# Performance work log

Measured on AMD Instinct MI355X. Metric: run time of the kernel, lower is better.

## Reference

```python
import jax, jax.numpy as jnp
import numpy as np
import math

PERIODS = [4, 2, 1]          # period_num[-3:] sorted desc
SEQ, PRED, CH = 192, 96, 8
TOPM, DM = 20, 512
N_TRAIN, BSZ = 10000, 32


def decompose_mg(data):
    # data: [N, L, C] -> mg: [P, N, L, C], offset-removed (last step per period)
    N, L, C = data.shape
    mgs = []
    for g in PERIODS:
        cur = data.reshape(N, L // g, g, C).mean(axis=2)   # pooled
        cur = jnp.repeat(cur, g, axis=1)                   # repeat_interleave
        mgs.append(cur)
    mg = jnp.stack(mgs, axis=0)                            # [P, N, L, C]
    offset = mg[:, :, -1:, :]
    return mg - offset


def l2norm(x, eps=1e-12):
    n = jnp.sqrt(jnp.sum(x * x, axis=-1, keepdims=True))
    return x / jnp.maximum(n, eps)


def setup_inputs() -> dict:
    key = jax.random.key(0)
    ks = jax.random.split(key, 10)
    F = SEQ * CH
    return {
        "x": jax.random.normal(ks[0], (BSZ, SEQ, CH), dtype=jnp.float32),
        "index": jax.random.randint(ks[1], (BSZ,), 0, N_TRAIN),
        "train_data_all": jax.random.normal(ks[2], (N_TRAIN, SEQ, CH), dtype=jnp.float32),
        "y_data_all": jax.random.normal(ks[3], (N_TRAIN, PRED, CH), dtype=jnp.float32),
        "W_sim": jax.random.normal(ks[4], (F, F), dtype=jnp.float32) / math.sqrt(F),
        "b_sim": jax.random.normal(ks[5], (F,), dtype=jnp.float32) * 0.01,
        "Wq": jax.random.normal(ks[6], (CH, DM), dtype=jnp.float32) / math.sqrt(CH),
        "bq": jax.random.normal(ks[7], (DM,), dtype=jnp.float32) * 0.01,
        "Wk": jax.random.normal(ks[8], (CH, DM), dtype=jnp.float32) / math.sqrt(CH),
        "bk": jax.random.normal(ks[9], (DM,), dtype=jnp.float32) * 0.01,
    }


def reference(x, index, train_data_all, y_data_all, W_sim, b_sim, Wq, bq, Wk, bk):
    P = len(PERIODS)
    bsz = x.shape[0]
    n_train = train_data_all.shape[0]

    # multi-period decomposition (prepare_dataset + retrieve)
    train_mg = decompose_mg(train_data_all)   # [P, N, SEQ, CH]
    y_mg = decompose_mg(y_data_all)           # [P, N, PRED, CH]
    x_mg = decompose_mg(x)                    # [P, B, SEQ, CH]

    # periodic_batch_corr: shared linear then cosine similarity
    bx = x_mg.reshape(P, bsz, -1) @ W_sim + b_sim           # [P, B, F]
    ax = train_mg.reshape(P, n_train, -1) @ W_sim + b_sim   # [P, N, F]
    sim = jnp.einsum('pbf,pnf->pbn', l2norm(bx), l2norm(ax))

    # self-exclusion sliding mask (train=True)
    win = 2 * (SEQ + PRED) - 1
    slid = jnp.arange(win)[None, :] + (index - SEQ - PRED + 1)[:, None]
    slid = jnp.clip(slid, 0, n_train - 1)
    mask = jnp.zeros((bsz, n_train), dtype=bool).at[
        jnp.arange(bsz)[:, None], slid].set(True)
    sim = jnp.where(mask[None], -jnp.inf, sim)

    # top-m retrieval
    _, topm_idx = jax.lax.top_k(sim, TOPM)                  # [P, B, TOPM]

    # gather neighbors per period
    gather = jax.vmap(lambda src, i: src[i])                # over period axis
    k = gather(train_mg, topm_idx)                          # [P, B, M, SEQ, CH]
    v = gather(y_mg, topm_idx)                              # [P, B, M, PRED, CH]

    # cross attention (shared projections across periods)
    q_emb = x_mg @ Wq + bq                                  # [P, B, S, D]
    k_emb = k @ Wk + bk                                     # [P, B, M, T, D]
    scores = jnp.einsum('pbsd,pbmtd->pbsmt', q_emb, k_emb) / math.sqrt(DM)
    S = scores.shape[2]
    w = jax.nn.softmax(scores.reshape(P, bsz, S, TOPM * S), axis=-1)
    w = w.reshape(P, bsz, S, TOPM, S)
    nw = w.sum(axis=-1).sum(axis=2)                         # [P, B, M]
    nw = jax.nn.softmax(nw, axis=-1)
    out = jnp.einsum('pbm,pbmlc->pblc', nw, v)              # [P, B, PRED, CH]
    return out
```

## Files before the change

### kernel.cpp

```cpp
#include <hip/hip_runtime.h>
#include <hip/hip_bf16.h>
#include <math.h>

#define NPER 3
#define SEQL 192
#define PREDL 96
#define CH 8
#define FD 1536
#define NT 10000
#define BS 32
#define PB 96
#define TOPM 20
#define DM 512
#define HALFW 287
#define NROWS 30000
#define NRP2 10112
#define NRB2 79
#define NCB 12
#define PCOLS 24
#define NWG2 (NRB2*NCB)
#define NJ 3840
#define K0R 384
#define K1R 768
#define K2R 1536
#define KS 16
#define NCH 4
#define CHSZ (NT/NCH)
#define NWTG 4080
#define NB_DOT (3*NRB2)
#define BUFSZ (2*128*32)
#define RSQRT_DM 0.04419417382415922f

typedef __attribute__((ext_vector_type(8))) short bf16x8;
typedef __attribute__((ext_vector_type(4))) float f32x4;
typedef __attribute__((address_space(3))) short lds_short_t;
typedef __attribute__((address_space(1))) const short glb_short_t;

__device__ inline float bflo(unsigned u){ return __uint_as_float(u << 16); }
__device__ inline float bfhi(unsigned u){ return __uint_as_float(u & 0xFFFF0000u); }
__device__ inline float bf2f(unsigned short u){ return __uint_as_float((unsigned)u << 16); }
__device__ inline unsigned short f2bf(float v){
  __hip_bfloat16 h = __float2bfloat16(v);
  return *reinterpret_cast<unsigned short*>(&h);
}

template<int L>
__device__ __forceinline__ void dec_body(const float* __restrict__ data,
                                         float* __restrict__ mg,
                                         __hip_bfloat16* __restrict__ m0,
                                         __hip_bfloat16* __restrict__ m1,
                                         __hip_bfloat16* __restrict__ m2,
                                         __hip_bfloat16* __restrict__ trH,
                                         __hip_bfloat16* __restrict__ trL,
                                         int N, int n, float* fpool) {
  float* row = fpool;
  float* m4  = fpool + L*CH;
  float* m2s = fpool + L*CH + (L/4)*CH;
  const float* src = data + (size_t)n*L*CH;
  for (int e = threadIdx.x; e < L*CH/4; e += 256)
    *reinterpret_cast<float4*>(&row[e*4]) = *reinterpret_cast<const float4*>(&src[e*4]);
  __syncthreads();
  for (int i = threadIdx.x; i < (L/4)*CH; i += 256) {
    int j = i >> 3, c = i & 7;
    m4[i] = (row[(4*j)*CH+c] + row[(4*j+1)*CH+c] + row[(4*j+2)*CH+c] + row[(4*j+3)*CH+c]) * 0.25f;
  }
  for (int i = threadIdx.x; i < (L/2)*CH; i += 256) {
    int j = i >> 3, c = i & 7;
    m2s[i] = (row[(2*j)*CH+c] + row[(2*j+1)*CH+c]) * 0.5f;
  }
  __syncthreads();
  if (mg) {
    size_t plane = (size_t)N*L*CH;
    size_t base  = (size_t)n*L*CH;
    for (int e = threadIdx.x; e < L*CH/4; e += 256) {
      int i = e*4;
      int l = i >> 3, c0 = i & 7;
      float v0[4], v1[4], v2[4];
      #pragma unroll
      for (int j=0;j<4;j++) {
        int c = c0 + j;
        v0[j] = m4[(l>>2)*CH+c] - m4[(L/4-1)*CH+c];
        v1[j] = m2s[(l>>1)*CH+c] - m2s[(L/2-1)*CH+c];
        v2[j] = row[i+j] - row[(L-1)*CH+c];
      }
      *reinterpret_cast<float4*>(&mg[base+i])           = make_float4(v0[0],v0[1],v0[2],v0[3]);
      *reinterpret_cast<float4*>(&mg[plane+base+i])     = make_float4(v1[0],v1[1],v1[2],v1[3]);
      *reinterpret_cast<float4*>(&mg[2*plane+base+i])   = make_float4(v2[0],v2[1],v2[2],v2[3]);
    }
  }
  if (m0) {
    unsigned short* p0 = (unsigned short*)m0 + (size_t)n*K0R;
    unsigned short* p1 = (unsigned short*)m1 + (size_t)n*K1R;
    unsigned short* p2 = (unsigned short*)m2 + (size_t)n*K2R;
    for (int e = threadIdx.x; e < K0R/4; e += 256) {
      int i = e*4, c0 = i & 7;
      ushort4 u;
      u.x = f2bf(m4[i]   - m4[(L/4-1)*CH + c0]);
      u.y = f2bf(m4[i+1] - m4[(L/4-1)*CH + c0+1]);
      u.z = f2bf(m4[i+2] - m4[(L/4-1)*CH + c0+2]);
      u.w = f2bf(m4[i+3] - m4[(L/4-1)*CH + c0+3]);
      *reinterpret_cast<ushort4*>(&p0[i]) = u;
    }
    for (int e = threadIdx.x; e < K1R/4; e += 256) {
      int i = e*4, c0 = i & 7;
      ushort4 u;
      u.x = f2bf(m2s[i]   - m2s[(L/2-1)*CH + c0]);
      u.y = f2bf(m2s[i+1] - m2s[(L/2-1)*CH + c0+1]);
      u.z = f2bf(m2s[i+2] - m2s[(L/2-1)*CH + c0+2]);
      u.w = f2bf(m2s[i+3] - m2s[(L/2-1)*CH + c0+3]);
      *reinterpret_cast<ushort4*>(&p1[i]) = u;
    }
    for (int e = threadIdx.x; e < K2R/4; e += 256) {
      int i = e*4, c0 = i & 7;
      ushort4 u;
      u.x = f2bf(row[i]   - row[(L-1)*CH + c0]);
      u.y = f2bf(row[i+1] - row[(L-1)*CH + c0+1]);
      u.z = f2bf(row[i+2] - row[(L-1)*CH + c0+2]);
      u.w = f2bf(row[i+3] - row[(L-1)*CH + c0+3]);
      *reinterpret_cast<ushort4*>(&p2[i]) = u;
    }
  }
  if (trH) {
    unsigned short* h = (unsigned short*)trH + (size_t)n*L*CH;
    unsigned short* l = (unsigned short*)trL + (size_t)n*L*CH;
    for (int e = threadIdx.x; e < L*CH/4; e += 256) {
      int i = e*4;
      ushort4 uh, ul;
      uh.x = f2bf(row[i]);   ul.x = f2bf(row[i]   - bf2f(uh.x));
      uh.y = f2bf(row[i+1]); ul.y = f2bf(row[i+1] - bf2f(uh.y));
      uh.z = f2bf(row[i+2]); ul.z = f2bf(row[i+2] - bf2f(uh.z));
      uh.w = f2bf(row[i+3]); ul.w = f2bf(row[i+3] - bf2f(uh.w));
      *reinterpret_cast<ushort4*>(&h[i]) = uh;
      *reinterpret_cast<ushort4*>(&l[i]) = ul;
    }
  }
}

__device__ __forceinline__ void wtg_body(const float* __restrict__ W,
                                         __hip_bfloat16* __restrict__ wt0,
                                         __hip_bfloat16* __restrict__ wt1,
                                         __hip_bfloat16* __restrict__ wt2,
                                         const float* __restrict__ Wq,
                                         const float* __restrict__ bq,
                                         const float* __restrict__ Wk,
                                         const float* __restrict__ bk,
                                         float* __restrict__ cst,
                                         int wb, float* fpool) {
  int bxx = wb / 48, byy = wb % 48;
  if (bxx == 84) {
    if (byy != 0) return;
    int tt = threadIdx.x;
    if (tt < 64) {
      int c = tt >> 3, e = tt & 7;
      float s = 0.f;
      for (int d=0; d<DM; d++) s += Wq[c*DM+d] * Wk[e*DM+d];
      cst[tt] = s;
    } else if (tt < 72) {
      int c = tt - 64; float s=0.f;
      for (int d=0;d<DM;d++) s += Wq[c*DM+d]*bk[d];
      cst[tt] = s;
    } else if (tt < 80) {
      int e = tt - 72; float s=0.f;
      for (int d=0;d<DM;d++) s += Wk[e*DM+d]*bq[d];
      cst[tt] = s;
    } else if (tt == 80) {
      float s=0.f;
      for (int d=0;d<DM;d++) s += bq[d]*bk[d];
      cst[80] = s;
    }
    return;
  }
  int G, kr0, Kred;
  __hip_bfloat16* Wt;
  if (bxx < 12)      { G = 4; kr0 = bxx*32;      Kred = K0R; Wt = wt0; }
  else if (bxx < 36) { G = 2; kr0 = (bxx-12)*32; Kred = K1R; Wt = wt1; }
  else               { G = 1; kr0 = (bxx-36)*32; Kred = K2R; Wt = wt2; }
  int f0 = byy*32;
  int k0 = kr0*G;
  int tid = threadIdx.x, tx = tid & 31, ty = tid >> 5;
  for (int i = ty; i < 32*G; i += 8)
    fpool[i*33 + tx] = W[(size_t)(k0+i)*FD + f0 + tx];
  __syncthreads();
  for (int fl = ty; fl < 32; fl += 8) {
    float s = 0.f;
    for (int i=0;i<G;i++) s += fpool[(((tx>>3)*G+i)*8 + (tx&7))*33 + fl];
    Wt[(size_t)(f0+fl)*Kred + kr0 + tx] = __float2bfloat16(s);
  }
}

__global__ __launch_bounds__(256) void k_front(const float* __restrict__ x,
                                               const float* __restrict__ train,
                                               float* __restrict__ x_mg,
                                               __hip_bfloat16* __restrict__ m0,
                                               __hip_bfloat16* __restrict__ m1,
                                               __hip_bfloat16* __restrict__ m2,
                                               __hip_bfloat16* __restrict__ trH,
                                               __hip_bfloat16* __restrict__ trL,
                                               const float* __restrict__ W,
                                               __hip_bfloat16* __restrict__ wt0,
                                               __hip_bfloat16* __restrict__ wt1,
                                               __hip_bfloat16* __restrict__ wt2,
                                               const float* __restrict__ Wq,
                                               const float* __restrict__ bq,
                                               const float* __restrict__ Wk,
                                               const float* __restrict__ bk,
                                               float* __restrict__ cst) {
  __shared__ float fpool[128*33];
  int bid = blockIdx.x;
  if (bid < NT) {
    dec_body<SEQL>(train, nullptr, m0, m1, m2, trH, trL, NT, bid, fpool);
  } else if (bid < NT + NWTG) {
    wtg_body(W, wt0, wt1, wt2, Wq, bq, Wk, bk, cst, bid - NT, fpool);
  } else {
    dec_body<SEQL>(x, x_mg, nullptr, nullptr, nullptr, nullptr, nullptr,
                   BS, bid - NT - NWTG, fpool);
  }
}

__global__ __launch_bounds__(256) void k_bx_part(const float* __restrict__ xmg,
                                                 const float* __restrict__ W,
                                                 float* __restrict__ bxp) {
  __shared__ float xs[PB][17];
  __shared__ float Ws[16][65];
  int f0 = blockIdx.x * 64;
  int ks = blockIdx.y;
  int kbase = ks * (FD/KS);
  int tid = threadIdx.x;
  int fl = tid & 63, gp = tid >> 6;
  float acc[24];
  #pragma unroll
  for (int j=0;j<24;j++) acc[j]=0.f;
  for (int k0 = kbase; k0 < kbase + FD/KS; k0 += 16) {
    for (int e = tid; e < PB*16; e += 256) {
      int r = e >> 4, k = e & 15;
      xs[r][k] = xmg[(size_t)r*FD + k0 + k];
    }
    for (int e = tid; e < 16*64; e += 256) {
      int k = e >> 6, f = e & 63;
      Ws[k][f] = W[(size_t)(k0+k)*FD + f0 + f];
    }
    __syncthreads();
    #pragma unroll
    for (int kk = 0; kk < 16; kk++) {
      float w = Ws[kk][fl];
      #pragma unroll
      for (int j=0;j<24;j++) acc[j] += w * xs[gp + 4*j][kk];
    }
    __syncthreads();
  }
  #pragma unroll
  for (int j=0;j<24;j++) {
    int pb = gp + 4*j;
    bxp[((size_t)ks*PB + pb)*FD + f0 + fl] = acc[j];
  }
}

__global__ __launch_bounds__(256) void k_bxnorm(const float* __restrict__ bxp,
                                                const float* __restrict__ bsim,
                                                float* __restrict__ u_out,
                                                float* __restrict__ cpb) {
  __shared__ float rowv[FD];
  __shared__ float r1[256], r2[256];
  __shared__ float invs;
  int pb = blockIdx.x, tid = threadIdx.x;
  float s2 = 0.f, sb = 0.f;
  for (int f = tid; f < FD; f += 256) {
    float s = 0.f;
    #pragma unroll
    for (int ks=0; ks<KS; ks++) s += bxp[((size_t)ks*PB + pb)*FD + f];
    s += bsim[f];
    rowv[f] = s;
    s2 += s*s; sb += s*bsim[f];
  }
  r1[tid]=s2; r2[tid]=sb; __syncthreads();
  for (int off=128; off>0; off>>=1) {
    if (tid<off) { r1[tid]+=r1[tid+off]; r2[tid]+=r2[tid+off]; }
    __syncthreads();
  }
  if (tid==0) {
    float iv = 1.f / fmaxf(sqrtf(r1[0]), 1e-12f);
    invs = iv;
    cpb[pb] = r2[0] * iv;
  }
  __syncthreads();
  float iv = invs;
  for (int f = tid; f < FD; f += 256) u_out[(size_t)pb*FD + f] = rowv[f]*iv;
}

__global__ __launch_bounds__(256) void k_t_part(const float* __restrict__ u,
                                                const float* __restrict__ W,
                                                float* __restrict__ tp) {
  __shared__ float us[PB][17];
  __shared__ float Wt[64][17];
  int k0 = blockIdx.x * 64;
  int ks = blockIdx.y;
  int fbase = ks * (FD/KS);
  int tid = threadIdx.x;
  int kl = tid & 63, gp = tid >> 6;
  float acc[24];
  #pragma unroll
  for (int j=0;j<24;j++) acc[j]=0.f;
  for (int fc = fbase; fc < fbase + FD/KS; fc += 16) {
    for (int e = tid; e < PB*16; e += 256) {
      int r = e >> 4, f = e & 15;
      us[r][f] = u[(size_t)r*FD + fc + f];
    }
    for (int e = tid; e < 64*16; e += 256) {
      int k = e >> 4, f = e & 15;
      Wt[k][f] = W[(size_t)(k0+k)*FD + fc + f];
    }
    __syncthreads();
    #pragma unroll
    for (int ff = 0; ff < 16; ff++) {
      float w = Wt[kl][ff];
      #pragma unroll
      for (int j=0;j<24;j++) acc[j] += w * us[gp + 4*j][ff];
    }
    __syncthreads();
  }
  #pragma unroll
  for (int j=0;j<24;j++) {
    int pb = gp + 4*j;
    tp[((size_t)ks*PB + pb)*FD + k0 + kl] = acc[j];
  }
}

__global__ __launch_bounds__(192) void k_tred_adj(const float* __restrict__ tp,
                                                  __hip_bfloat16* __restrict__ tadjH,
                                                  __hip_bfloat16* __restrict__ tadjL) {
  __shared__ float ts[SEQL*CH];
  __shared__ float Tc[CH];
  int pb = blockIdx.x;
  int p = pb / BS;
  int g = (p==0) ? 4 : (p==1) ? 2 : 1;
  int l = threadIdx.x;
  #pragma unroll
  for (int c=0;c<CH;c++) {
    float s = 0.f;
    #pragma unroll
    for (int ks=0; ks<KS; ks++) s += tp[((size_t)ks*PB + pb)*FD + l*CH + c];
    ts[l*CH+c] = s;
  }
  __syncthreads();
  if (l < CH) {
    float s=0.f;
    for (int j=0;j<SEQL;j++) s += ts[j*CH+l];
    Tc[l] = s;
  }
  __syncthreads();
  int j0 = (l/g)*g;
  bool last = (j0 == SEQL-g);
  float ig = 1.f/(float)g;
  unsigned short* th = (unsigned short*)tadjH;
  unsigned short* tl = (unsigned short*)tadjL;
  #pragma unroll
  for (int c=0;c<CH;c++) {
    float s = 0.f;
    for (int jj=0;jj<g;jj++) s += ts[(j0+jj)*CH+c];
    float v = s*ig - (last ? Tc[c]*ig : 0.f);
    unsigned short hv = f2bf(v);
    th[(size_t)pb*FD + l*CH+c] = hv;
    tl[(size_t)pb*FD + l*CH+c] = f2bf(v - bf2f(hv));
  }
}

__device__ __forceinline__ void norm_body(const short* __restrict__ A,
                                          const short* __restrict__ B,
                                          int K, int p, int seg,
                                          const float* __restrict__ bsim,
                                          float* __restrict__ part,
                                          short* pool) {
  int q = NWG2 >> 3, r = NWG2 & 7;
  int xcd = seg & 7, pos = seg >> 3;
  int wgid = (xcd < r ? xcd*(q+1) : r*(q+1) + (xcd-r)*q) + pos;
  int rb = wgid / NCB, cb = wgid - rb*NCB;
  int row0 = rb*128, col0 = cb*128;
  int tid = threadIdx.x, lane = tid & 63, wid = tid >> 6;
  int wr = (wid>>1)*64, wc = (wid&1)*64;

  size_t aoff[2], boff[2];
  int ldsb[2];
  #pragma unroll
  for (int i=0;i<2;i++) {
    int lrow = (wid*2+i)*16 + (lane>>2);
    int sl = lane & 3;
    int ss = (sl - lrow - (lrow>>2)) & 3;
    aoff[i] = (size_t)(row0 + lrow)*K + 8*ss;
    boff[i] = (size_t)(col0 + lrow)*K + 8*ss;
    ldsb[i] = (wid*2+i)*16*32;
  }

  f32x4 acc[4][4];
  #pragma unroll
  for (int m=0;m<4;m++)
    #pragma unroll
    for (int n=0;n<4;n++) acc[m][n] = (f32x4){0.f,0.f,0.f,0.f};

  int kslot = lane >> 4;
  #pragma unroll
  for (int i=0;i<2;i++) {
    __builtin_amdgcn_global_load_lds((glb_short_t*)(A + aoff[i]),
                                     (lds_short_t*)&pool[ldsb[i]], 16, 0, 0);
    __builtin_amdgcn_global_load_lds((glb_short_t*)(B + boff[i]),
                                     (lds_short_t*)&pool[128*32 + ldsb[i]], 16, 0, 0);
  }
  __syncthreads();
  int cur = 0;
  for (int k0 = 0; k0 < K; k0 += 32) {
    if (k0 + 32 < K) {
      short* nb = pool + (cur^1)*BUFSZ;
      #pragma unroll
      for (int i=0;i<2;i++) {
        __builtin_amdgcn_global_load_lds((glb_short_t*)(A + aoff[i] + k0 + 32),
                                         (lds_short_t*)&nb[ldsb[i]], 16, 0, 0);
        __builtin_amdgcn_global_load_lds((glb_short_t*)(B + boff[i] + k0 + 32),
                                         (lds_short_t*)&nb[128*32 + ldsb[i]], 16, 0, 0);
      }
    }
    const short* lA = pool + cur*BUFSZ;
    const short* lB = pool + cur*BUFSZ + 128*32;
    bf16x8 af[4], bfr[4];
    #pragma unroll
    for (int m=0;m<4;m++) {
      int rr = wr + m*16 + (lane&15);
      int s = (kslot + rr + (rr>>2)) & 3;
      af[m] = *(const bf16x8*)&lA[rr*32 + s*8];
    }
    #pragma unroll
    for (int n=0;n<4;n++) {
      int rr = wc + n*16 + (lane&15);
      int s = (kslot + rr + (rr>>2)) & 3;
      bfr[n] = *(const bf16x8*)&lB[rr*32 + s*8];
    }
    #pragma unroll
    for (int m=0;m<4;m++)
      #pragma unroll
      for (int n=0;n<4;n++)
        acc[m][n] = __builtin_amdgcn_mfma_f32_16x16x32_bf16(af[m], bfr[n], acc[m][n], 0, 0, 0);
    __syncthreads();
    cur ^= 1;
  }

  float bv[4];
  #pragma unroll
  for (int n=0;n<4;n++) bv[n] = bsim[col0 + wc + n*16 + (lane&15)];
  int pslot = cb*2 + (wid&1);
  #pragma unroll
  for (int m=0;m<4;m++) {
    #pragma unroll
    for (int j=0;j<4;j++) {
      float s = 0.f;
      #pragma unroll
      for (int n=0;n<4;n++) { float v = acc[m][n][j] + bv[n]; s += v*v; }
      s += __shfl_xor(s, 1); s += __shfl_xor(s, 2);
      s += __shfl_xor(s, 4); s += __shfl_xor(s, 8);
      if ((lane & 15) == 0) {
        int rr = row0 + wr + m*16 + (lane>>4)*4 + j;
        part[((size_t)p*NRP2 + rr)*PCOLS + pslot] = s;
      }
    }
  }
}

__device__ __forceinline__ void dot_body(const short* __restrict__ A,
                                         const short* __restrict__ B,
                                         float* __restrict__ dst,
                                         int cbn, short* pool) {
  int col0 = cbn * 128;
  int tid = threadIdx.x, lane = tid & 63, wid = tid >> 6;
  int wr = (wid>>1)*64, wc = (wid&1)*64;

  size_t aoff[2], boff[2];
  int ldsb[2];
  #pragma unroll
  for (int i=0;i<2;i++) {
    int lrow = (wid*2+i)*16 + (lane>>2);
    int sl = lane & 3;
    int ss = (sl - lrow - (lrow>>2)) & 3;
    aoff[i] = (size_t)lrow*FD + 8*ss;
    boff[i] = (size_t)(col0 + lrow)*FD + 8*ss;
    ldsb[i] = (wid*2+i)*16*32;
  }

  f32x4 acc[4][4];
  #pragma unroll
  for (int m=0;m<4;m++)
    #pragma unroll
    for (int n=0;n<4;n++) acc[m][n] = (f32x4){0.f,0.f,0.f,0.f};

  int kslot = lane >> 4;
  #pragma unroll
  for (int i=0;i<2;i++) {
    __builtin_amdgcn_global_load_lds((glb_short_t*)(A + aoff[i]),
                                     (lds_short_t*)&pool[ldsb[i]], 16, 0, 0);
    __builtin_amdgcn_global_load_lds((glb_short_t*)(B + boff[i]),
                                     (lds_short_t*)&pool[128*32 + ldsb[i]], 16, 0, 0);
  }
  __syncthreads();
  int cur = 0;
  for (int k0 = 0; k0 < FD; k0 += 32) {
    if (k0 + 32 < FD) {
      short* nb = pool + (cur^1)*BUFSZ;
      #pragma unroll
      for (int i=0;i<2;i++) {
        __builtin_amdgcn_global_load_lds((glb_short_t*)(A + aoff[i] + k0 + 32),
                                         (lds_short_t*)&nb[ldsb[i]], 16, 0, 0);
        __builtin_amdgcn_global_load_lds((glb_short_t*)(B + boff[i] + k0 + 32),
                                         (lds_short_t*)&nb[128*32 + ldsb[i]], 16, 0, 0);
      }
    }
    const short* lA = pool + cur*BUFSZ;
    const short* lB = pool + cur*BUFSZ + 128*32;
    bf16x8 af[4], bfr[4];
    #pragma unroll
    for (int m=0;m<4;m++) {
      int rr = wr + m*16 + (lane&15);
      int s = (kslot + rr + (rr>>2)) & 3;
      af[m] = *(const bf16x8*)&lA[rr*32 + s*8];
    }
    #pragma unroll
    for (int n=0;n<4;n++) {
      int rr = wc + n*16 + (lane&15);
      int s = (kslot + rr + (rr>>2)) & 3;
      bfr[n] = *(const bf16x8*)&lB[rr*32 + s*8];
    }
    #pragma unroll
    for (int m=0;m<4;m++)
      #pragma unroll
      for (int n=0;n<4;n++)
        acc[m][n] = __builtin_amdgcn_mfma_f32_16x16x32_bf16(af[m], bfr[n], acc[m][n], 0, 0, 0);
    __syncthreads();
    cur ^= 1;
  }

  #pragma unroll
  for (int m=0;m<4;m++) {
    int prow = wr + m*16 + (lane>>4)*4;
    if (prow >= PB) continue;
    #pragma unroll
    for (int n=0;n<4;n++) {
      int ncol = col0 + wc + n*16 + (lane&15);
      if (ncol >= NT) continue;
      #pragma unroll
      for (int j=0;j<4;j++) {
        dst[(size_t)(prow + j)*NT + ncol] = acc[m][n][j];
      }
    }
  }
}

__global__ __launch_bounds__(256) void k_gemms(
    const __hip_bfloat16* __restrict__ A0b, const __hip_bfloat16* __restrict__ A1b,
    const __hip_bfloat16* __restrict__ A2b,
    const __hip_bfloat16* __restrict__ B0b, const __hip_bfloat16* __restrict__ B1b,
    const __hip_bfloat16* __restrict__ B2b,
    const float* __restrict__ bsim, float* __restrict__ part,
    const __hip_bfloat16* __restrict__ tadjHb, const __hip_bfloat16* __restrict__ tadjLb,
    const __hip_bfloat16* __restrict__ trHb, const __hip_bfloat16* __restrict__ trLb,
    float* __restrict__ dotp3) {
  __shared__ __align__(16) short pool[2*BUFSZ];
  int bid = blockIdx.x;
  if (bid < NB_DOT) {
    int term = bid / NRB2, cbn = bid - term*NRB2;
    const short* A = (term == 2) ? (const short*)tadjLb : (const short*)tadjHb;
    const short* B = (term == 1) ? (const short*)trLb   : (const short*)trHb;
    dot_body(A, B, dotp3 + (size_t)term*PB*NT, cbn, pool);
  } else if (bid < NB_DOT + NWG2) {
    norm_body((const short*)A2b, (const short*)B2b, K2R, 2, bid - NB_DOT, bsim, part, pool);
  } else if (bid < NB_DOT + 2*NWG2) {
    norm_body((const short*)A1b, (const short*)B1b, K1R, 1, bid - NB_DOT - NWG2, bsim, part, pool);
  } else {
    norm_body((const short*)A0b, (const short*)B0b, K0R, 0,
              bid - NB_DOT - 2*NWG2, bsim, part, pool);
  }
}

__global__ __launch_bounds__(256) void k_topk_part(const float* __restrict__ dotp3,
                                                   const float* __restrict__ cpb,
                                                   const float* __restrict__ part,
                                                   const int* __restrict__ index,
                                                   float* __restrict__ cv,
                                                   int* __restrict__ ci) {
  __shared__ float vals[CHSZ];
  __shared__ float rv[4];
  __shared__ int   ri[4];
  int pb = blockIdx.x, ch = blockIdx.y;
  int p = pb / BS, b = pb - p*BS;
  int n0 = ch*CHSZ;
  int tid = threadIdx.x, lane = tid & 63, wv = tid >> 6;
  int idx = index[b];
  int bl = idx - HALFW; if (bl < 0) bl = 0;
  int bh = idx + HALFW; if (bh > NT-1) bh = NT-1;
  float cp = cpb[pb];
  for (int i = tid; i < CHSZ; i += 256) {
    int n = n0 + i;
    const float* pr = &part[((size_t)p*NRP2 + n)*PCOLS];
    float s2 = 0.f;
    #pragma unroll
    for (int cb2=0; cb2<PCOLS; cb2++) s2 += pr[cb2];
    float d = dotp3[(size_t)pb*NT + n]
            + dotp3[(size_t)PB*NT + (size_t)pb*NT + n]
            + dotp3[2*(size_t)PB*NT + (size_t)pb*NT + n] + cp;
    float v = d / fmaxf(sqrtf(s2), 1e-12f);
    if (n >= bl && n <= bh) v = -INFINITY;
    vals[i] = v;
  }
  __syncthreads();
  for (int it = 0; it < TOPM; it++) {
    float bv = -INFINITY; int bi = CHSZ;
    for (int i = tid; i < CHSZ; i += 256) {
      float v = vals[i];
      if (v > bv) { bv = v; bi = i; }
    }
    #pragma unroll
    for (int off=32; off>0; off>>=1) {
      float ov = __shfl_xor(bv, off);
      int   oi = __shfl_xor(bi, off);
      if (ov > bv || (ov == bv && oi < bi)) { bv = ov; bi = oi; }
    }
    if (lane == 0) { rv[wv] = bv; ri[wv] = bi; }
    __syncthreads();
    if (tid == 0) {
      float fv = rv[0]; int fi = ri[0];
      #pragma unroll
      for (int w2=1; w2<4; w2++)
        if (rv[w2] > fv || (rv[w2] == fv && ri[w2] < fi)) { fv = rv[w2]; fi = ri[w2]; }
      cv[(pb*NCH + ch)*TOPM + it] = fv;
      ci[(pb*NCH + ch)*TOPM + it] = n0 + fi;
      vals[fi] = -INFINITY;
    }
    __syncthreads();
  }
}

__global__ __launch_bounds__(64) void k_topk_merge(const float* __restrict__ cv,
                                                   const int* __restrict__ ci,
                                                   int* __restrict__ topm) {
  __shared__ float v[NCH*TOPM];
  __shared__ int   id[NCH*TOPM];
  int pb = blockIdx.x;
  int lane = threadIdx.x;
  for (int i = lane; i < NCH*TOPM; i += 64) {
    v[i]  = cv[pb*NCH*TOPM + i];
    id[i] = ci[pb*NCH*TOPM + i];
  }
  __syncthreads();
  for (int it = 0; it < TOPM; it++) {
    float bv = -INFINITY; int bi = 0x7fffffff;
    for (int i = lane; i < NCH*TOPM; i += 64) {
      float vv = v[i];
      int ii = id[i];
      if (vv > bv || (vv == bv && ii < bi)) { bv = vv; bi = ii; }
    }
    #pragma unroll
    for (int off=32; off>0; off>>=1) {
      float ov = __shfl_xor(bv, off);
      int   oi = __shfl_xor(bi, off);
      if (ov > bv || (ov == bv && oi < bi)) { bv = ov; bi = oi; }
    }
    if (lane == 0) topm[pb*TOPM + it] = bi;
    for (int i = lane; i < NCH*TOPM; i += 64)
      if (id[i] == bi) v[i] = -INFINITY;
    __syncthreads();
  }
}

__device__ __forceinline__ void v_body(const float* __restrict__ ydata,
                                       const int* __restrict__ topm,
                                       float* __restrict__ vbuf,
                                       int bm, float* bpool) {
  float* row = bpool;
  float* m4  = bpool + 768;
  float* m2  = bpool + 960;
  int pb = bm / TOPM;
  int p = pb / BS;
  int n = topm[bm];
  int tid = threadIdx.x;
  const float* src = ydata + (size_t)n*PREDL*CH;
  for (int i=tid; i<PREDL*CH; i+=256) row[i]=src[i];
  __syncthreads();
  for (int i=tid; i<(PREDL/4)*CH; i+=256) {
    int j=i>>3, c=i&7;
    m4[i] = (row[(4*j)*CH+c]+row[(4*j+1)*CH+c]+row[(4*j+2)*CH+c]+row[(4*j+3)*CH+c])*0.25f;
  }
  for (int i=tid; i<(PREDL/2)*CH; i+=256) {
    int j=i>>3, c=i&7;
    m2[i] = (row[(2*j)*CH+c]+row[(2*j+1)*CH+c])*0.5f;
  }
  __syncthreads();
  float* dst = vbuf + (size_t)bm*PREDL*CH;
  for (int i=tid; i<PREDL*CH; i+=256) {
    int l=i>>3, c=i&7;
    float v;
    if (p==0)      v = m4[(l>>2)*CH+c] - m4[(PREDL/4-1)*CH+c];
    else if (p==1) v = m2[(l>>1)*CH+c] - m2[(PREDL/2-1)*CH+c];
    else           v = row[i] - row[(PREDL-1)*CH+c];
    dst[i] = v;
  }
}

template<int SH>
__device__ __forceinline__ void scores_body(
    const short* __restrict__ plane, int Kp,
    int pb, int sg,
    const int* __restrict__ topm,
    const float* __restrict__ xmg,
    const float* __restrict__ cst,
    float* __restrict__ nws,
    float* sc, int* tl, float* wred, float* lcst) {
  constexpr int UNQ = SEQL >> SH;
  constexpr int J   = TOPM * UNQ;
  constexpr int NU  = (J + 255) >> 8;
  constexpr bool FULL = (J % 256 == 0);
  int tid = threadIdx.x;
  int lane = tid & 63, wv = tid >> 6;
  if (tid < TOPM) tl[tid] = topm[pb*TOPM + tid];
  if (tid >= 32 && tid < 32+81) lcst[tid-32] = cst[tid-32];
  __syncthreads();
  uint4 kreg[NU];
  #pragma unroll
  for (int u=0; u<NU; u++) {
    int j = tid + u*256;
    if (FULL || j < J) {
      int m = j / UNQ, jj = j - m*UNQ;
      kreg[u] = *reinterpret_cast<const uint4*>(plane + (size_t)tl[m]*Kp + jj*8);
    }
  }
  for (int s8 = 0; s8 < 8; s8++) {
    int s = sg*8 + s8;
    int qr = pb*SEQL + s;
    float4 qa = *reinterpret_cast<const float4*>(&xmg[(size_t)qr*8]);
    float4 qc = *reinterpret_cast<const float4*>(&xmg[(size_t)qr*8+4]);
    float xq[8] = {qa.x,qa.y,qa.z,qa.w,qc.x,qc.y,qc.z,qc.w};
    float q[8];
    #pragma unroll
    for (int e=0;e<8;e++) {
      float ss = lcst[72+e];
      #pragma unroll
      for (int c=0;c<8;c++) ss += xq[c]*lcst[c*8+e];
      q[e] = ss;
    }
    float qb_s = lcst[80];
    #pragma unroll
    for (int c=0;c<8;c++) qb_s += xq[c]*lcst[64+c];
    float ms[NU];
    float lmax = -INFINITY;
    #pragma unroll
    for (int u=0; u<NU; u++) {
      int j = tid + u*256;
      if (FULL || j < J) {
        uint4 w = kreg[u];
        float s0 = qb_s;
        s0 += q[0]*bflo(w.x) + q[1]*bfhi(w.x);
        s0 += q[2]*bflo(w.y) + q[3]*bfhi(w.y);
        s0 += q[4]*bflo(w.z) + q[5]*bfhi(w.z);
        s0 += q[6]*bflo(w.w) + q[7]*bfhi(w.w);
        s0 *= RSQRT_DM;
        ms[u] = s0;
        lmax = fmaxf(lmax, s0);
      } else ms[u] = -INFINITY;
    }
    #pragma unroll
    for (int off=32; off>0; off>>=1) lmax = fmaxf(lmax, __shfl_xor(lmax, off));
    if (lane==0) wred[wv] = lmax;
    __syncthreads();
    float mx = fmaxf(fmaxf(wred[0],wred[1]),fmaxf(wred[2],wred[3]));
    float lsum = 0.f;
    #pragma unroll
    for (int u=0; u<NU; u++) {
      int j = tid + u*256;
      if (FULL || j < J) {
        float e = __expf(ms[u]-mx);
        sc[j] = e;
        lsum += e;
      }
    }
    #pragma unroll
    for (int off=32; off>0; off>>=1) lsum += __shfl_xor(lsum, off);
    if (lane==0) wred[4+wv] = lsum;
    __syncthreads();
    float invZ = 1.f / (wred[4]+wred[5]+wred[6]+wred[7]);
    for (int m = wv; m < TOPM; m += 4) {
      float v = 0.f;
      #pragma unroll
      for (int jj = 0; jj < UNQ; jj += 64) {
        int j2 = jj + lane;
        if (UNQ % 64 == 0 || j2 < UNQ) v += sc[m*UNQ + j2];
      }
      #pragma unroll
      for (int off=32; off>0; off>>=1) v += __shfl_xor(v, off);
      if (lane==0) nws[((size_t)pb*SEQL + s)*TOPM + m] = v * invZ;
    }
    __syncthreads();
  }
}

__global__ __launch_bounds__(256) void k_back(const __hip_bfloat16* __restrict__ m0,
                                              const __hip_bfloat16* __restrict__ m1,
                                              const __hip_bfloat16* __restrict__ m2,
                                              const int* __restrict__ topm,
                                              const float* __restrict__ xmg,
                                              const float* __restrict__ cst,
                                              float* __restrict__ nws,
                                              const float* __restrict__ ydata,
                                              float* __restrict__ vbuf) {
  __shared__ float bpool[3968];
  int bid = blockIdx.x;
  if (bid < PB*24) {
    int pb = bid / 24, sg = bid - (bid/24)*24;
    int p = pb / BS;
    float* sc = bpool;
    int* tl = (int*)(bpool + 3840);
    float* wred = bpool + 3864;
    float* lcst = bpool + 3872;
    if (p == 0)
      scores_body<2>((const short*)m0, K0R, pb, sg, topm, xmg, cst, nws, sc, tl, wred, lcst);
    else if (p == 1)
      scores_body<1>((const short*)m1, K1R, pb, sg, topm, xmg, cst, nws, sc, tl, wred, lcst);
    else
      scores_body<0>((const short*)m2, K2R, pb, sg, topm, xmg, cst, nws, sc, tl, wred, lcst);
  } else {
    v_body(ydata, topm, vbuf, bid - PB*24, bpool);
  }
}

__global__ __launch_bounds__(256) void k_out(const float* __restrict__ nws,
                                             const float* __restrict__ vbuf,
                                             float* __restrict__ out) {
  __shared__ float nwp[TOPM];
  __shared__ float nwf[TOPM];
  int pb = blockIdx.x;
  int tid = threadIdx.x;
  if (tid < TOPM) {
    float s=0.f;
    for (int ss=0; ss<SEQL; ss++) s += nws[((size_t)pb*SEQL+ss)*TOPM + tid];
    nwp[tid] = s;
  }
  __syncthreads();
  if (tid==0) {
    float mx=-INFINITY;
    for (int m=0;m<TOPM;m++) mx=fmaxf(mx,nwp[m]);
    float Z=0.f;
    for (int m=0;m<TOPM;m++){ float e=expf(nwp[m]-mx); nwf[m]=e; Z+=e; }
    float iz=1.f/Z;
    for (int m=0;m<TOPM;m++) nwf[m]*=iz;
  }
  __syncthreads();
  for (int i=tid; i<PREDL*CH; i+=256) {
    float o=0.f;
    #pragma unroll
    for (int m=0;m<TOPM;m++) o += nwf[m]*vbuf[((size_t)pb*TOPM+m)*PREDL*CH + i];
    out[(size_t)pb*PREDL*CH + i] = o;
  }
}

extern "C" void kernel_launch(void* const* d_in, const int* in_sizes, int n_in,
                              void* d_out, int out_size, void* d_ws, size_t ws_size,
                              hipStream_t stream) {
  const float* x     = (const float*)d_in[0];
  const int*   index = (const int*)  d_in[1];
  const float* train = (const float*)d_in[2];
  const float* ydata = (const float*)d_in[3];
  const float* Wsim  = (const float*)d_in[4];
  const float* bsim  = (const float*)d_in[5];
  const float* Wq    = (const float*)d_in[6];
  const float* bq    = (const float*)d_in[7];
  const float* Wk    = (const float*)d_in[8];
  const float* bk    = (const float*)d_in[9];
  float* out = (float*)d_out;

  float* ws = (float*)d_ws;
  size_t off = 0;
  auto alloc = [&](size_t n)->float* { float* pp = ws + off; off += (n + 63) & ~(size_t)63; return pp; };
  __hip_bfloat16* m0b = (__hip_bfloat16*)alloc((size_t)NRP2*K0R/2);
  __hip_bfloat16* m1b = (__hip_bfloat16*)alloc((size_t)NRP2*K1R/2);
  __hip_bfloat16* m2b = (__hip_bfloat16*)alloc((size_t)NRP2*K2R/2);
  __hip_bfloat16* wt0 = (__hip_bfloat16*)alloc((size_t)FD*K0R/2);
  __hip_bfloat16* wt1 = (__hip_bfloat16*)alloc((size_t)FD*K1R/2);
  __hip_bfloat16* wt2 = (__hip_bfloat16*)alloc((size_t)FD*K2R/2);
  __hip_bfloat16* trH = (__hip_bfloat16*)alloc((size_t)NRP2*FD/2);
  __hip_bfloat16* trL = (__hip_bfloat16*)alloc((size_t)NRP2*FD/2);
  __hip_bfloat16* tadjH = (__hip_bfloat16*)alloc((size_t)128*FD/2);
  __hip_bfloat16* tadjL = (__hip_bfloat16*)alloc((size_t)128*FD/2);
  float* x_mg     = alloc((size_t)NPER*BS*FD);
  float* bx       = alloc((size_t)PB*FD);
  float* cpb      = alloc(PB);
  float* gpart    = alloc((size_t)KS*PB*FD);
  float* part     = alloc((size_t)NPER*NRP2*PCOLS);
  float* dotp3    = alloc((size_t)3*PB*NT);
  float* cv       = alloc((size_t)PB*NCH*TOPM);
  int*   ci       = (int*)alloc(PB*NCH*TOPM);
  int*   topm     = (int*)alloc(PB*TOPM);
  float* cst      = alloc(128);
  float* vbuf     = alloc((size_t)PB*TOPM*PREDL*CH);
  float* nws      = alloc((size_t)PB*SEQL*TOPM);
  if (off * sizeof(float) > ws_size) return;

  k_front<<<NT + NWTG + BS, 256, 0, stream>>>(x, train, x_mg, m0b, m1b, m2b, trH, trL,
                                              Wsim, wt0, wt1, wt2, Wq, bq, Wk, bk, cst);
  k_bx_part<<<dim3(24, KS), 256, 0, stream>>>(x_mg, Wsim, gpart);
  k_bxnorm<<<PB, 256, 0, stream>>>(gpart, bsim, bx, cpb);
  k_t_part<<<dim3(24, KS), 256, 0, stream>>>(bx, Wsim, gpart);
  k_tred_adj<<<PB, 192, 0, stream>>>(gpart, tadjH, tadjL);
  k_gemms<<<NB_DOT + 3*NWG2, 256, 0, stream>>>(m0b, m1b, m2b, wt0, wt1, wt2, bsim, part,
                                               tadjH, tadjL, trH, trL, dotp3);
  k_topk_part<<<dim3(PB, NCH), 256, 0, stream>>>(dotp3, cpb, part, index, cv, ci);
  k_topk_merge<<<PB, 64, 0, stream>>>(cv, ci, topm);
  k_back<<<PB*24 + PB*TOPM, 256, 0, stream>>>(m0b, m1b, m2b, topm, x_mg, cst, nws,
                                              ydata, vbuf);
  k_out<<<PB, 256, 0, stream>>>(nws, vbuf, out);
}
```

Before: 412.8 us.

## Triple-buffer LDS tiles in GEMM bodies with partial vmcnt waits

Both GEMM bodies (norm_body and dot_body) move from a double-buffered to a triple-buffered LDS pipeline. Global-to-LDS loads are issued two k-tiles ahead, and each barrier waits only until the older tile has landed (s_waitcnt vmcnt(4)) rather than for every outstanding load. This hides more global-memory latency behind MFMA work. In exchange, LDS per block grows by half, which may reduce how many blocks fit per CU, and the hand-written waitcnt/barrier sequence depends on correct counting of outstanding loads.

```diff
diff --git a/kernel.cpp b/kernel.cpp
--- a/kernel.cpp
+++ b/kernel.cpp
@@ -364,6 +364,13 @@
   }
 }
 
+#define PIPE_SYNC_4()  do { asm volatile("s_waitcnt vmcnt(4)" ::: "memory"); \
+                            __builtin_amdgcn_s_barrier(); \
+                            __builtin_amdgcn_sched_barrier(0); } while(0)
+#define PIPE_SYNC_0()  do { asm volatile("s_waitcnt vmcnt(0)" ::: "memory"); \
+                            __builtin_amdgcn_s_barrier(); \
+                            __builtin_amdgcn_sched_barrier(0); } while(0)
+
 __device__ __forceinline__ void norm_body(const short* __restrict__ A,
                                           const short* __restrict__ B,
                                           int K, int p, int seg,
@@ -397,6 +404,7 @@
     for (int n=0;n<4;n++) acc[m][n] = (f32x4){0.f,0.f,0.f,0.f};
 
   int kslot = lane >> 4;
+  int nt = K >> 5;
   #pragma unroll
   for (int i=0;i<2;i++) {
     __builtin_amdgcn_global_load_lds((glb_short_t*)(A + aoff[i]),
@@ -404,21 +412,30 @@
     __builtin_amdgcn_global_load_lds((glb_short_t*)(B + boff[i]),
                                      (lds_short_t*)&pool[128*32 + ldsb[i]], 16, 0, 0);
   }
-  __syncthreads();
+  #pragma unroll
+  for (int i=0;i<2;i++) {
+    __builtin_amdgcn_global_load_lds((glb_short_t*)(A + aoff[i] + 32),
+                                     (lds_short_t*)&pool[BUFSZ + ldsb[i]], 16, 0, 0);
+    __builtin_amdgcn_global_load_lds((glb_short_t*)(B + boff[i] + 32),
+                                     (lds_short_t*)&pool[BUFSZ + 128*32 + ldsb[i]], 16, 0, 0);
+  }
+  PIPE_SYNC_4();
   int cur = 0;
-  for (int k0 = 0; k0 < K; k0 += 32) {
-    if (k0 + 32 < K) {
-      short* nb = pool + (cur^1)*BUFSZ;
+  for (int t = 0; t < nt; ++t) {
+    if (t + 2 < nt) {
+      int nx = cur + 2; if (nx >= 3) nx -= 3;
+      short* nb = pool + nx*BUFSZ;
+      int kn = (t+2) << 5;
       #pragma unroll
       for (int i=0;i<2;i++) {
-        __builtin_amdgcn_global_load_lds((glb_short_t*)(A + aoff[i] + k0 + 32),
+        __builtin_amdgcn_global_load_lds((glb_short_t*)(A + aoff[i] + kn),
                                          (lds_short_t*)&nb[ldsb[i]], 16, 0, 0);
-        __builtin_amdgcn_global_load_lds((glb_short_t*)(B + boff[i] + k0 + 32),
+        __builtin_amdgcn_global_load_lds((glb_short_t*)(B + boff[i] + kn),
                                          (lds_short_t*)&nb[128*32 + ldsb[i]], 16, 0, 0);
       }
     }
     const short* lA = pool + cur*BUFSZ;
-    const short* lB = pool + cur*BUFSZ + 128*32;
+    const short* lB = lA + 128*32;
     bf16x8 af[4], bfr[4];
     #pragma unroll
     for (int m=0;m<4;m++) {
@@ -437,8 +454,10 @@
       #pragma unroll
       for (int n=0;n<4;n++)
         acc[m][n] = __builtin_amdgcn_mfma_f32_16x16x32_bf16(af[m], bfr[n], acc[m][n], 0, 0, 0);
-    __syncthreads();
-    cur ^= 1;
+    if (t + 1 < nt) {
+      if (t + 2 < nt) PIPE_SYNC_4(); else PIPE_SYNC_0();
+    }
+    cur = (cur + 1 == 3) ? 0 : cur + 1;
   }
 
   float bv[4];
@@ -489,6 +508,7 @@
     for (int n=0;n<4;n++) acc[m][n] = (f32x4){0.f,0.f,0.f,0.f};
 
   int kslot = lane >> 4;
+  const int nt = FD >> 5;
   #pragma unroll
   for (int i=0;i<2;i++) {
     __builtin_amdgcn_global_load_lds((glb_short_t*)(A + aoff[i]),
@@ -496,21 +516,30 @@
     __builtin_amdgcn_global_load_lds((glb_short_t*)(B + boff[i]),
                                      (lds_short_t*)&pool[128*32 + ldsb[i]], 16, 0, 0);
   }
-  __syncthreads();
+  #pragma unroll
+  for (int i=0;i<2;i++) {
+    __builtin_amdgcn_global_load_lds((glb_short_t*)(A + aoff[i] + 32),
+                                     (lds_short_t*)&pool[BUFSZ + ldsb[i]], 16, 0, 0);
+    __builtin_amdgcn_global_load_lds((glb_short_t*)(B + boff[i] + 32),
+                                     (lds_short_t*)&pool[BUFSZ + 128*32 + ldsb[i]], 16, 0, 0);
+  }
+  PIPE_SYNC_4();
   int cur = 0;
-  for (int k0 = 0; k0 < FD; k0 += 32) {
-    if (k0 + 32 < FD) {
-      short* nb = pool + (cur^1)*BUFSZ;
+  for (int t = 0; t < nt; ++t) {
+    if (t + 2 < nt) {
+      int nx = cur + 2; if (nx >= 3) nx -= 3;
+      short* nb = pool + nx*BUFSZ;
+      int kn = (t+2) << 5;
       #pragma unroll
       for (int i=0;i<2;i++) {
-        __builtin_amdgcn_global_load_lds((glb_short_t*)(A + aoff[i] + k0 + 32),
+        __builtin_amdgcn_global_load_lds((glb_short_t*)(A + aoff[i] + kn),
                                          (lds_short_t*)&nb[ldsb[i]], 16, 0, 0);
-        __builtin_amdgcn_global_load_lds((glb_short_t*)(B + boff[i] + k0 + 32),
+        __builtin_amdgcn_global_load_lds((glb_short_t*)(B + boff[i] + kn),
                                          (lds_short_t*)&nb[128*32 + ldsb[i]], 16, 0, 0);
       }
     }
     const short* lA = pool + cur*BUFSZ;
-    const short* lB = pool + cur*BUFSZ + 128*32;
+    const short* lB = lA + 128*32;
     bf16x8 af[4], bfr[4];
     #pragma unroll
     for (int m=0;m<4;m++) {
@@ -529,8 +558,10 @@
       #pragma unroll
       for (int n=0;n<4;n++)
         acc[m][n] = __builtin_amdgcn_mfma_f32_16x16x32_bf16(af[m], bfr[n], acc[m][n], 0, 0, 0);
-    __syncthreads();
-    cur ^= 1;
+    if (t + 1 < nt) {
+      if (t + 2 < nt) PIPE_SYNC_4(); else PIPE_SYNC_0();
+    }
+    cur = (cur + 1 == 3) ? 0 : cur + 1;
   }
 
   #pragma unroll
@@ -558,7 +589,7 @@
     const __hip_bfloat16* __restrict__ tadjHb, const __hip_bfloat16* __restrict__ tadjLb,
     const __hip_bfloat16* __restrict__ trHb, const __hip_bfloat16* __restrict__ trLb,
     float* __restrict__ dotp3) {
-  __shared__ __align__(16) short pool[2*BUFSZ];
+  __shared__ __align__(16) short pool[3*BUFSZ];
   int bid = blockIdx.x;
   if (bid < NB_DOT) {
     int term = bid / NRB2, cbn = bid - term*NRB2;
```

New measurement: 406.1 us. About the same (-1.6%).
